# Kernel tuning notes

Measured on AMD Instinct MI355X. Metric: run time of the kernel, lower is better.

Reference implementation:

```python
import jax, jax.numpy as jnp
import numpy as np

DIM = 1024
EPS = 1e-5

def layernorm(x, g, b):
    m = jnp.mean(x, axis=-1, keepdims=True)
    v = jnp.var(x, axis=-1, keepdims=True)
    return (x - m) / jnp.sqrt(v + EPS) * g + b

def setup_inputs() -> dict:
    key = jax.random.key(0)
    ks = jax.random.split(key, 12)
    B, L, D = 4, 2048, DIM
    s = 1.0 / np.sqrt(D)
    return {
        "q": jax.random.normal(ks[0], (B, L, D), jnp.float32),
        "k": jax.random.normal(ks[1], (B, L, D), jnp.float32),
        "v": jax.random.normal(ks[2], (B, L, D), jnp.float32),
        "gq": jnp.ones((D,), jnp.float32), "bq": jnp.zeros((D,), jnp.float32),
        "gk": jnp.ones((D,), jnp.float32), "bk": jnp.zeros((D,), jnp.float32),
        "gv": jnp.ones((D,), jnp.float32), "bv": jnp.zeros((D,), jnp.float32),
        "Wq": jax.random.uniform(ks[3], (D, D), jnp.float32, -s, s),
        "Wk": jax.random.uniform(ks[4], (D, D), jnp.float32, -s, s),
        "Wv": jax.random.uniform(ks[5], (D, D), jnp.float32, -s, s),
        "Wp": jax.random.uniform(ks[6], (D, D), jnp.float32, -s, s),
        "bp": jax.random.uniform(ks[7], (D,), jnp.float32, -s, s),
    }

def reference(q, k, v, gq, bq, gk, bk, gv, bv, Wq, Wk, Wv, Wp, bp):
    scale = DIM ** -0.5
    qn = layernorm(q, gq, bq) @ Wq.T  # [B,Q,D]
    kn = layernorm(k, gk, bk) @ Wk.T  # [B,K,D]
    vn = layernorm(v, gv, bv) @ Wv.T  # [B,K,D]
    attn = jnp.einsum('bqc,bkc->bqk', qn, kn)
    attn = jax.nn.relu(attn) * scale  # ReLU on raw scores, then scale (matches in-place *=)
    attn_mask = jax.nn.softmax(attn, axis=-1)
    out = jnp.einsum('bqk,bkc->bqc', attn_mask, vn)
    out = out @ Wp.T + bp
    return (attn, out)
```

## Files before the change

### kernel.cpp

```cpp
#include <hip/hip_runtime.h>


typedef __attribute__((ext_vector_type(8))) short short8v;
typedef __attribute__((ext_vector_type(4))) float f32x4;

#define DEVI __device__ __forceinline__

DEVI float b2f(unsigned short u) {
  union { unsigned int i; float f; } x;
  x.i = ((unsigned int)u) << 16;
  return x.f;
}
DEVI unsigned short f2b(float f) {
  union { float f; unsigned int i; } x;
  x.f = f;
  unsigned int r = x.i + 0x7fffu + ((x.i >> 16) & 1u);
  return (unsigned short)(r >> 16);
}

DEVI bool sniff_bf16(const unsigned short* wq) {
  int bad = 0;
#pragma unroll
  for (int j = 0; j < 64; ++j) bad |= (fabsf(b2f(wq[j])) > 0.0625f) ? 1 : 0;
  return bad == 0;
}

DEVI void async16(const unsigned short* g, unsigned short* l) {
  __builtin_amdgcn_global_load_lds(
      (const __attribute__((address_space(1))) void*)g,
      (__attribute__((address_space(3))) void*)l, 16, 0, 0);
}

DEVI void wait_lgkm0() { asm volatile("s_waitcnt lgkmcnt(0)" ::: "memory"); }
DEVI void wait_lgkm8() { asm volatile("s_waitcnt lgkmcnt(8)" ::: "memory"); }
template <int N> DEVI void wait_vm();
template <> DEVI void wait_vm<0>() { asm volatile("s_waitcnt vmcnt(0)" ::: "memory"); }
template <> DEVI void wait_vm<6>() { asm volatile("s_waitcnt vmcnt(6)" ::: "memory"); }

DEVI void stage_q(const unsigned short* G, int ld, unsigned short* L,
                  int w, int lane, int k0) {
  int r8 = lane >> 3;
  int scol = ((lane & 7) ^ r8) * 8;
  async16(G + (size_t)(w * 8 + r8) * ld + k0 + scol, L + (w * 8) * 64);
}
DEVI void stage_half(const unsigned short* G, int ld, unsigned short* L,
                     int w, int lane, int k0) {
  stage_q(G, ld, L, w, lane, k0);
  stage_q(G + (size_t)64 * ld, ld, L + 64 * 64, w, lane, k0);
}

template <int NB>
DEVI void gemm8_core(unsigned short* sA, unsigned short* sB,
                     const unsigned short* Ab, const unsigned short* Bb,
                     int m0, int n0, int lda, int ldb, int K, int tid,
                     f32x4 (&acc)[8][2 * NB]) {
  int lane = tid & 63, w = tid >> 6;
  int wm = w >> 2, wn = w & 3;
  int l15 = lane & 15, quad = lane >> 4;
  int rxor = l15 & 7;
  int cb0 = (quad ^ rxor) * 8;
  int cb1 = ((4 + quad) ^ rxor) * 8;
  const int nst = K >> 6;
  const int BSZ = NB * 128 * 64;
  const unsigned short* A_ = Ab + (size_t)m0 * lda;
  const unsigned short* B_ = Bb + (size_t)n0 * ldb;

  if constexpr (NB == 2) {
    const unsigned short* A0 = A_;
    const unsigned short* A1 = A_ + (size_t)128 * lda;
    const unsigned short* B0g = B_;
    const unsigned short* B1g = B_ + (size_t)128 * ldb;
    stage_half(A0, lda, sA, w, lane, 0);
    stage_half(A1, lda, sA + 8192, w, lane, 0);
    stage_half(B0g, ldb, sB, w, lane, 0);
    stage_half(B1g, ldb, sB + 8192, w, lane, 0);
    if (nst > 1) {
      stage_half(A0, lda, sA + 16384, w, lane, 64);
      stage_half(A1, lda, sA + 16384 + 8192, w, lane, 64);
      stage_half(B0g, ldb, sB + 16384, w, lane, 64);
      wait_vm<6>();
    } else {
      wait_vm<0>();
    }
    __builtin_amdgcn_s_barrier();

    for (int t = 0; t < nst; ++t) {
      const int b = t & 1, nb2 = b ^ 1;
      const unsigned short* rA = sA + b * 16384 + (wm * 128 + l15) * 64;
      const unsigned short* rB = sB + b * 16384 + (wn * 64 + l15) * 64;
      short8v a03[4][2], a47[4][2], b01[2][2], b23[2][2];

#pragma unroll
      for (int mt = 0; mt < 4; ++mt) {
        a03[mt][0] = *(const short8v*)(rA + mt * 1024 + cb0);
        a03[mt][1] = *(const short8v*)(rA + mt * 1024 + cb1);
      }
#pragma unroll
      for (int nt = 0; nt < 2; ++nt) {
        b01[nt][0] = *(const short8v*)(rB + nt * 1024 + cb0);
        b01[nt][1] = *(const short8v*)(rB + nt * 1024 + cb1);
      }
      if (t + 1 < nst)
        stage_half(B1g, ldb, sB + nb2 * 16384 + 8192, w, lane, (t + 1) << 6);
      wait_lgkm8();
      __builtin_amdgcn_s_barrier();
      wait_lgkm0();
      __builtin_amdgcn_sched_barrier(0);
      __builtin_amdgcn_s_setprio(1);
#pragma unroll
      for (int mt = 0; mt < 4; ++mt)
#pragma unroll
        for (int nt = 0; nt < 2; ++nt) {
          acc[mt][nt] = __builtin_amdgcn_mfma_f32_16x16x32_bf16(a03[mt][0], b01[nt][0], acc[mt][nt], 0, 0, 0);
          acc[mt][nt] = __builtin_amdgcn_mfma_f32_16x16x32_bf16(a03[mt][1], b01[nt][1], acc[mt][nt], 0, 0, 0);
        }
      __builtin_amdgcn_s_setprio(0);
      __builtin_amdgcn_s_barrier();

#pragma unroll
      for (int mt = 0; mt < 4; ++mt) {
        a47[mt][0] = *(const short8v*)(rA + (4 + mt) * 1024 + cb0);
        a47[mt][1] = *(const short8v*)(rA + (4 + mt) * 1024 + cb1);
      }
      __builtin_amdgcn_s_barrier();
      wait_lgkm0();
      __builtin_amdgcn_sched_barrier(0);
      __builtin_amdgcn_s_setprio(1);
#pragma unroll
      for (int mt = 0; mt < 4; ++mt)
#pragma unroll
        for (int nt = 0; nt < 2; ++nt) {
          acc[4 + mt][nt] = __builtin_amdgcn_mfma_f32_16x16x32_bf16(a47[mt][0], b01[nt][0], acc[4 + mt][nt], 0, 0, 0);
          acc[4 + mt][nt] = __builtin_amdgcn_mfma_f32_16x16x32_bf16(a47[mt][1], b01[nt][1], acc[4 + mt][nt], 0, 0, 0);
        }
      __builtin_amdgcn_s_setprio(0);
      __builtin_amdgcn_s_barrier();

#pragma unroll
      for (int nt = 0; nt < 2; ++nt) {
        b23[nt][0] = *(const short8v*)(rB + (2 + nt) * 1024 + cb0);
        b23[nt][1] = *(const short8v*)(rB + (2 + nt) * 1024 + cb1);
      }
      if (t + 2 < nst)
        stage_half(A0, lda, sA + b * 16384, w, lane, (t + 2) << 6);
      __builtin_amdgcn_s_barrier();
      wait_lgkm0();
      __builtin_amdgcn_sched_barrier(0);
      __builtin_amdgcn_s_setprio(1);
#pragma unroll
      for (int mt = 0; mt < 4; ++mt)
#pragma unroll
        for (int nt = 0; nt < 2; ++nt) {
          acc[mt][2 + nt] = __builtin_amdgcn_mfma_f32_16x16x32_bf16(a03[mt][0], b23[nt][0], acc[mt][2 + nt], 0, 0, 0);
          acc[mt][2 + nt] = __builtin_amdgcn_mfma_f32_16x16x32_bf16(a03[mt][1], b23[nt][1], acc[mt][2 + nt], 0, 0, 0);
        }
      __builtin_amdgcn_s_setprio(0);
      __builtin_amdgcn_s_barrier();

      if (t + 2 < nst) {
        stage_half(A1, lda, sA + b * 16384 + 8192, w, lane, (t + 2) << 6);
        stage_half(B0g, ldb, sB + b * 16384, w, lane, (t + 2) << 6);
      }
      __builtin_amdgcn_s_setprio(1);
#pragma unroll
      for (int mt = 0; mt < 4; ++mt)
#pragma unroll
        for (int nt = 0; nt < 2; ++nt) {
          acc[4 + mt][2 + nt] = __builtin_amdgcn_mfma_f32_16x16x32_bf16(a47[mt][0], b23[nt][0], acc[4 + mt][2 + nt], 0, 0, 0);
          acc[4 + mt][2 + nt] = __builtin_amdgcn_mfma_f32_16x16x32_bf16(a47[mt][1], b23[nt][1], acc[4 + mt][2 + nt], 0, 0, 0);
        }
      __builtin_amdgcn_s_setprio(0);
      if (t + 2 < nst) wait_vm<6>();
      else if (t + 1 < nst) wait_vm<0>();
      __builtin_amdgcn_s_barrier();
    }
  } else {
    stage_q(A_, lda, sA, w, lane, 0);
    stage_q(A_ + (size_t)128 * lda, lda, sA + 128 * 64, w, lane, 0);
    stage_half(B_, ldb, sB, w, lane, 0);
    stage_q(A_ + (size_t)64 * lda, lda, sA + 64 * 64, w, lane, 0);
    stage_q(A_ + (size_t)192 * lda, lda, sA + 192 * 64, w, lane, 0);
    if (nst > 1) {
      stage_q(A_, lda, sA + 16384, w, lane, 64);
      stage_q(A_ + (size_t)128 * lda, lda, sA + 16384 + 128 * 64, w, lane, 64);
      stage_half(B_, ldb, sB + BSZ, w, lane, 64);
    }
    for (int t = 0; t < nst; ++t) {
      const int b = t & 1;
      const unsigned short* rA = sA + b * 16384 + (wm * 128 + l15) * 64;
      const unsigned short* rB = sB + b * BSZ + (wn * 32 + l15) * 64;
      short8v a[4][2], bb[2][2];
      if (t + 1 < nst) {
        int kn = (t + 1) << 6;
        stage_q(A_ + (size_t)64 * lda, lda, sA + (b ^ 1) * 16384 + 64 * 64, w, lane, kn);
        stage_q(A_ + (size_t)192 * lda, lda, sA + (b ^ 1) * 16384 + 192 * 64, w, lane, kn);
        wait_vm<6>();
      } else {
        wait_vm<0>();
      }
      __builtin_amdgcn_s_barrier();
#pragma unroll
      for (int mt = 0; mt < 4; ++mt) {
        a[mt][0] = *(const short8v*)(rA + mt * 1024 + cb0);
        a[mt][1] = *(const short8v*)(rA + mt * 1024 + cb1);
      }
#pragma unroll
      for (int nt = 0; nt < 2; ++nt) {
        bb[nt][0] = *(const short8v*)(rB + nt * 1024 + cb0);
        bb[nt][1] = *(const short8v*)(rB + nt * 1024 + cb1);
      }
      wait_lgkm0();
      __builtin_amdgcn_sched_barrier(0);
      __builtin_amdgcn_s_setprio(1);
#pragma unroll
      for (int mt = 0; mt < 4; ++mt)
#pragma unroll
        for (int nt = 0; nt < 2; ++nt) {
          acc[mt][nt] = __builtin_amdgcn_mfma_f32_16x16x32_bf16(a[mt][0], bb[nt][0], acc[mt][nt], 0, 0, 0);
          acc[mt][nt] = __builtin_amdgcn_mfma_f32_16x16x32_bf16(a[mt][1], bb[nt][1], acc[mt][nt], 0, 0, 0);
        }
      __builtin_amdgcn_s_setprio(0);
      __builtin_amdgcn_s_barrier();
#pragma unroll
      for (int mt = 0; mt < 4; ++mt) {
        a[mt][0] = *(const short8v*)(rA + (4 + mt) * 1024 + cb0);
        a[mt][1] = *(const short8v*)(rA + (4 + mt) * 1024 + cb1);
      }
      if (t + 2 < nst) {
        int kn2 = (t + 2) << 6;
        stage_q(A_, lda, sA + b * 16384, w, lane, kn2);
        stage_q(A_ + (size_t)128 * lda, lda, sA + b * 16384 + 128 * 64, w, lane, kn2);
        stage_half(B_, ldb, sB + b * BSZ, w, lane, kn2);
      }
      __builtin_amdgcn_s_barrier();
      wait_lgkm0();
      __builtin_amdgcn_sched_barrier(0);
      __builtin_amdgcn_s_setprio(1);
#pragma unroll
      for (int mt = 0; mt < 4; ++mt)
#pragma unroll
        for (int nt = 0; nt < 2; ++nt) {
          acc[4 + mt][nt] = __builtin_amdgcn_mfma_f32_16x16x32_bf16(a[mt][0], bb[nt][0], acc[4 + mt][nt], 0, 0, 0);
          acc[4 + mt][nt] = __builtin_amdgcn_mfma_f32_16x16x32_bf16(a[mt][1], bb[nt][1], acc[4 + mt][nt], 0, 0, 0);
        }
      __builtin_amdgcn_s_setprio(0);
      __builtin_amdgcn_s_barrier();
    }
  }
}

DEVI int xcd_swz(int f, int nb) { return (f & 7) * (nb >> 3) + (f >> 3); }

struct PrepArgs {
  const void* q; const void* k; const void* v;
  const void* g[3]; const void* b[3];
  const void* W[4];
};

__global__ __launch_bounds__(256) void k_prep(PrepArgs pa,
    unsigned short* __restrict__ Wb, unsigned short* __restrict__ XN) {
  bool isbf = sniff_bf16((const unsigned short*)pa.W[0]);
  int bid = blockIdx.x, tid = threadIdx.x;
  if (bid < 2048) {
    int s = bid >> 9;
    size_t inner = ((size_t)(bid & 511)) * 2048 + (size_t)tid * 8;
    unsigned short* dst = Wb + (size_t)s * 1048576 + inner;
    if (isbf) {
      *(uint4*)dst = *(const uint4*)((const unsigned short*)pa.W[s] + inner);
    } else {
      const float* f = (const float*)pa.W[s] + inner;
      float4 a = *(const float4*)f;
      float4 b = *(const float4*)(f + 4);
      ushort4 o0 = { f2b(a.x), f2b(a.y), f2b(a.z), f2b(a.w) };
      ushort4 o1 = { f2b(b.x), f2b(b.y), f2b(b.z), f2b(b.w) };
      *(ushort4*)dst = o0;
      *(ushort4*)(dst + 4) = o1;
    }
  } else {
    int rb = bid - 2048;
    int wv = tid >> 6, lane = tid & 63;
    int row = rb * 4 + wv;
    int t = row >> 13;
    size_t r = (size_t)(row & 8191);
    const void* src = (t == 0) ? pa.q : (t == 1) ? pa.k : pa.v;
    float x[16];
    if (isbf) {
      const unsigned short* s = (const unsigned short*)src + r * 1024;
#pragma unroll
      for (int j = 0; j < 2; ++j) {
        uint4 pk = *(const uint4*)(s + j * 512 + lane * 8);
        const unsigned short* ps = (const unsigned short*)&pk;
#pragma unroll
        for (int e = 0; e < 8; ++e) x[j * 8 + e] = b2f(ps[e]);
      }
    } else {
      const float* s = (const float*)src + r * 1024;
#pragma unroll
      for (int j = 0; j < 4; ++j) {
        float4 pk = *(const float4*)(s + j * 256 + lane * 4);
        x[j * 4 + 0] = pk.x; x[j * 4 + 1] = pk.y;
        x[j * 4 + 2] = pk.z; x[j * 4 + 3] = pk.w;
      }
    }
    float s1 = 0.f, s2 = 0.f;
#pragma unroll
    for (int e = 0; e < 16; ++e) { s1 += x[e]; s2 += x[e] * x[e]; }
    for (int off = 32; off > 0; off >>= 1) {
      s1 += __shfl_xor(s1, off);
      s2 += __shfl_xor(s2, off);
    }
    float m  = s1 * (1.0f / 1024.0f);
    float m2 = s2 * (1.0f / 1024.0f);
    float rstd = rsqrtf(m2 - m * m + 1e-5f);
    unsigned short* dst = XN + (size_t)row * 1024;
    if (isbf) {
      const unsigned short* gp = (const unsigned short*)pa.g[t];
      const unsigned short* bp = (const unsigned short*)pa.b[t];
#pragma unroll
      for (int j = 0; j < 2; ++j) {
        uint4 gk = *(const uint4*)(gp + j * 512 + lane * 8);
        uint4 bk = *(const uint4*)(bp + j * 512 + lane * 8);
        const unsigned short* gs = (const unsigned short*)&gk;
        const unsigned short* bs = (const unsigned short*)&bk;
        uint4 out;
        unsigned short* os = (unsigned short*)&out;
#pragma unroll
        for (int e = 0; e < 8; ++e)
          os[e] = f2b((x[j * 8 + e] - m) * rstd * b2f(gs[e]) + b2f(bs[e]));
        *(uint4*)(dst + j * 512 + lane * 8) = out;
      }
    } else {
      const float* gp = (const float*)pa.g[t];
      const float* bp = (const float*)pa.b[t];
#pragma unroll
      for (int j = 0; j < 4; ++j) {
        float4 gk = *(const float4*)(gp + j * 256 + lane * 4);
        float4 bk = *(const float4*)(bp + j * 256 + lane * 4);
        ushort4 o;
        o.x = f2b((x[j * 4 + 0] - m) * rstd * gk.x + bk.x);
        o.y = f2b((x[j * 4 + 1] - m) * rstd * gk.y + bk.y);
        o.z = f2b((x[j * 4 + 2] - m) * rstd * gk.z + bk.z);
        o.w = f2b((x[j * 4 + 3] - m) * rstd * gk.w + bk.w);
        *(ushort4*)(dst + j * 256 + lane * 4) = o;
      }
    }
  }
}

__global__ __launch_bounds__(512, 2) void k_megaproj(
    const unsigned short* __restrict__ XN, const unsigned short* __restrict__ Wb,
    unsigned short* __restrict__ QN, unsigned short* __restrict__ VNT) {
  __shared__ __align__(16) unsigned short sA[2 * 256 * 64];
  __shared__ __align__(16) unsigned short sB[2 * 256 * 64];
  int x = xcd_swz((int)blockIdx.x, 384), tid = threadIdx.x;
  int lane = tid & 63, w = tid >> 6;
  int wm = w >> 2, wn = w & 3;
  int l15 = lane & 15, quad = lane >> 4;
  f32x4 acc[8][4];
#pragma unroll
  for (int i = 0; i < 8; ++i)
#pragma unroll
    for (int j = 0; j < 4; ++j) acc[i][j] = (f32x4){0.f, 0.f, 0.f, 0.f};

  unsigned short* C;
  int m0, n0, ldc;
  if (x < 256) {
    int t = x >> 7, i = x & 127;
    m0 = (i >> 2) * 256; n0 = (i & 3) * 256; ldc = 1024;
    gemm8_core<2>(sA, sB, XN + (size_t)t * 8388608, Wb + (size_t)t * 1048576,
                  m0, n0, 1024, 1024, 1024, tid, acc);
    C = QN + (size_t)t * 8388608;
  } else {
    int i = x - 256, z = i >> 5, j = i & 31;
    m0 = (j >> 3) * 256; n0 = (j & 7) * 256; ldc = 2048;
    gemm8_core<2>(sA, sB, Wb + 2 * 1048576, XN + 2 * 8388608 + (size_t)z * 2097152,
                  m0, n0, 1024, 1024, 1024, tid, acc);
    C = VNT + (size_t)z * 2097152;
  }
#pragma unroll
  for (int mt = 0; mt < 8; ++mt) {
    int mb = m0 + wm * 128 + mt * 16 + quad * 4;
#pragma unroll
    for (int nt = 0; nt < 4; ++nt) {
      int n = n0 + wn * 64 + nt * 16 + l15;
      f32x4 vc = acc[mt][nt];
#pragma unroll
      for (int r2 = 0; r2 < 4; ++r2) C[(size_t)(mb + r2) * ldc + n] = f2b(vc[r2]);
    }
  }
}

template <int EPI, int NB>
__global__ __launch_bounds__(512, 2) void k_gemm(
    const unsigned short* __restrict__ A, const unsigned short* __restrict__ B,
    void* __restrict__ Cv, long long coff,
    int K, int lda, int ldb, int ldc,
    long long sAb, long long sBb, long long sCb,
    float scale, const void* __restrict__ bias,
    const unsigned short* __restrict__ wq_sniff) {
  __shared__ __align__(16) unsigned short sA[2 * 256 * 64];
  __shared__ __align__(16) unsigned short sB[2 * NB * 128 * 64];
  int tid = threadIdx.x;
  int lane = tid & 63, w = tid >> 6;
  int wm = w >> 2, wn = w & 3;
  int l15 = lane & 15, quad = lane >> 4;

  int gx = gridDim.x, gy = gridDim.y;
  int nb = gx * gy * (int)gridDim.z;
  int f = (int)blockIdx.x + gx * ((int)blockIdx.y + gy * (int)blockIdx.z);
  f = xcd_swz(f, nb);
  int bx = f % gx;
  int rem = f / gx;
  int by = rem % gy;
  int bz = rem / gy;

  int m0 = by * 256, n0 = bx * (NB * 128);
  f32x4 acc[8][2 * NB];
#pragma unroll
  for (int i = 0; i < 8; ++i)
#pragma unroll
    for (int j = 0; j < 2 * NB; ++j) acc[i][j] = (f32x4){0.f, 0.f, 0.f, 0.f};

  gemm8_core<NB>(sA, sB, A + (long long)bz * sAb, B + (long long)bz * sBb,
                 m0, n0, lda, ldb, K, tid, acc);

  long long cbase = coff + (long long)bz * sCb;
  bool isbf = (EPI != 0) ? sniff_bf16(wq_sniff) : true;
#pragma unroll
  for (int mt = 0; mt < 8; ++mt) {
    int mb = m0 + wm * 128 + mt * 16 + quad * 4;
#pragma unroll
    for (int nt = 0; nt < 2 * NB; ++nt) {
      int n = n0 + wn * (NB * 32) + nt * 16 + l15;
      f32x4 vc = acc[mt][nt];
      if (EPI == 0) {
        unsigned short* C = (unsigned short*)Cv + cbase;
#pragma unroll
        for (int r2 = 0; r2 < 4; ++r2) C[(size_t)(mb + r2) * ldc + n] = f2b(vc[r2]);
      } else if (EPI == 1) {
        if (isbf) {
          unsigned short* C = (unsigned short*)Cv + cbase;
#pragma unroll
          for (int r2 = 0; r2 < 4; ++r2)
            C[(size_t)(mb + r2) * ldc + n] = f2b(fmaxf(vc[r2], 0.f) * scale);
        } else {
          float* C = (float*)Cv + cbase;
#pragma unroll
          for (int r2 = 0; r2 < 4; ++r2)
            C[(size_t)(mb + r2) * ldc + n] = fmaxf(vc[r2], 0.f) * scale;
        }
      } else {
        float bv2 = isbf ? b2f(((const unsigned short*)bias)[n])
                         : ((const float*)bias)[n];
        if (isbf) {
          unsigned short* C = (unsigned short*)Cv + cbase;
#pragma unroll
          for (int r2 = 0; r2 < 4; ++r2) C[(size_t)(mb + r2) * ldc + n] = f2b(vc[r2] + bv2);
        } else {
          float* C = (float*)Cv + cbase;
#pragma unroll
          for (int r2 = 0; r2 < 4; ++r2) C[(size_t)(mb + r2) * ldc + n] = vc[r2] + bv2;
        }
      }
    }
  }
}

__global__ __launch_bounds__(256) void k_softmax(const void* __restrict__ S,
    unsigned short* __restrict__ P, const unsigned short* __restrict__ wq_sniff) {
  bool isbf = sniff_bf16(wq_sniff);
  size_t row = blockIdx.x;
  int tid = threadIdx.x;
  float v[8];
  if (isbf) {
    const unsigned short* s = (const unsigned short*)S + row * 2048 + (size_t)tid * 8;
    ushort4 a = *(const ushort4*)s;
    ushort4 b = *(const ushort4*)(s + 4);
    v[0] = b2f(a.x); v[1] = b2f(a.y); v[2] = b2f(a.z); v[3] = b2f(a.w);
    v[4] = b2f(b.x); v[5] = b2f(b.y); v[6] = b2f(b.z); v[7] = b2f(b.w);
  } else {
    const float* s = (const float*)S + row * 2048 + (size_t)tid * 8;
    float4 a = *(const float4*)s;
    float4 b = *(const float4*)(s + 4);
    v[0] = a.x; v[1] = a.y; v[2] = a.z; v[3] = a.w;
    v[4] = b.x; v[5] = b.y; v[6] = b.z; v[7] = b.w;
  }
  float mx = v[0];
#pragma unroll
  for (int j = 1; j < 8; ++j) mx = fmaxf(mx, v[j]);
  for (int off = 32; off > 0; off >>= 1) mx = fmaxf(mx, __shfl_down(mx, off));
  __shared__ float sh[8];
  if ((tid & 63) == 0) sh[tid >> 6] = mx;
  __syncthreads();
  mx = fmaxf(fmaxf(sh[0], sh[1]), fmaxf(sh[2], sh[3]));
  float sum = 0.f;
#pragma unroll
  for (int j = 0; j < 8; ++j) { v[j] = __expf(v[j] - mx); sum += v[j]; }
  for (int off = 32; off > 0; off >>= 1) sum += __shfl_down(sum, off);
  if ((tid & 63) == 0) sh[4 + (tid >> 6)] = sum;
  __syncthreads();
  float inv = 1.0f / (sh[4] + sh[5] + sh[6] + sh[7]);
  ushort4 o0 = { f2b(v[0] * inv), f2b(v[1] * inv), f2b(v[2] * inv), f2b(v[3] * inv) };
  ushort4 o1 = { f2b(v[4] * inv), f2b(v[5] * inv), f2b(v[6] * inv), f2b(v[7] * inv) };
  unsigned short* p = P + row * 2048 + (size_t)tid * 8;
  *(ushort4*)p = o0;
  *(ushort4*)(p + 4) = o1;
}

static const size_t MB_ = 1024 * 1024;
static const size_t OFF_W   = 0;
static const size_t OFF_XN  = 8 * MB_ + 128 * 1024;
static const size_t OFF_QN  = OFF_XN + 48 * MB_;
static const size_t OFF_VNT = OFF_QN + 32 * MB_;
static const size_t OFF_P   = OFF_XN;
static const size_t OFF_O1  = OFF_XN + 32 * MB_;

extern "C" void kernel_launch(void* const* d_in, const int* in_sizes, int n_in,
                              void* d_out, int out_size, void* d_ws, size_t ws_size,
                              hipStream_t stream) {
  (void)in_sizes; (void)n_in; (void)out_size; (void)ws_size;
  char* ws = (char*)d_ws;
  unsigned short* Wb  = (unsigned short*)(ws + OFF_W);
  unsigned short* XN  = (unsigned short*)(ws + OFF_XN);
  unsigned short* QN  = (unsigned short*)(ws + OFF_QN);
  unsigned short* VNT = (unsigned short*)(ws + OFF_VNT);
  unsigned short* P   = (unsigned short*)(ws + OFF_P);
  unsigned short* O1  = (unsigned short*)(ws + OFF_O1);
  const unsigned short* WqS = (const unsigned short*)d_in[9];

  PrepArgs pa;
  pa.q = d_in[0]; pa.k = d_in[1]; pa.v = d_in[2];
  pa.g[0] = d_in[3]; pa.b[0] = d_in[4];
  pa.g[1] = d_in[5]; pa.b[1] = d_in[6];
  pa.g[2] = d_in[7]; pa.b[2] = d_in[8];
  pa.W[0] = d_in[9]; pa.W[1] = d_in[10]; pa.W[2] = d_in[11]; pa.W[3] = d_in[12];

  k_prep<<<8192, 256, 0, stream>>>(pa, Wb, XN);

  k_megaproj<<<384, 512, 0, stream>>>(XN, Wb, QN, VNT);

  k_gemm<1, 2><<<dim3(8, 8, 4), 512, 0, stream>>>(
      QN, QN + 8388608, d_out,
      0,
      1024, 1024, 1024, 2048,
      2097152LL, 2097152LL, 4194304LL,
      0.03125f, nullptr, WqS);

  k_softmax<<<8192, 256, 0, stream>>>(d_out, P, WqS);

  k_gemm<0, 1><<<dim3(8, 8, 4), 512, 0, stream>>>(
      P, VNT, O1,
      0,
      2048, 2048, 2048, 1024,
      4194304LL, 2097152LL, 2097152LL,
      0.f, nullptr, WqS);

  k_gemm<3, 1><<<dim3(8, 32, 1), 512, 0, stream>>>(
      O1, Wb + 3 * 1048576, d_out,
      16777216,
      1024, 1024, 1024, 1024,
      0LL, 0LL, 0LL,
      0.f, d_in[13], WqS);
}
```

Measured before the change: 404.4 us.

## Restructure GEMM main loop into single-barrier prefetch pipeline and split V projection tiles

Rewrites the shared gemm8_core software pipeline so each k-step issues the next stage's global-to-LDS loads up front, uses partial lgkmcnt waits between MFMA groups, and needs only one workgroup barrier per iteration instead of many. It also preloads the next stage's first fragments before the final MFMA block to hide LDS latency. Separately, the V projection in k_megaproj now uses 256x128 tiles (NB=1), raising its block count so the grid grows to 512 blocks, with XCD swizzle applied per branch. The risk is more register pressure from holding next-stage fragments, and less slack for the loads to land, since the loop waits for all outstanding loads (vmcnt 0) before its barrier each step.

```diff
diff --git a/kernel.cpp b/kernel.cpp
--- a/kernel.cpp
+++ b/kernel.cpp
@@ -31,11 +31,15 @@
       (__attribute__((address_space(3))) void*)l, 16, 0, 0);
 }
 
-DEVI void wait_lgkm0() { asm volatile("s_waitcnt lgkmcnt(0)" ::: "memory"); }
-DEVI void wait_lgkm8() { asm volatile("s_waitcnt lgkmcnt(8)" ::: "memory"); }
+template <int N> DEVI void wait_lgkm();
+template <> DEVI void wait_lgkm<0>() { asm volatile("s_waitcnt lgkmcnt(0)" ::: "memory"); }
+template <> DEVI void wait_lgkm<4>() { asm volatile("s_waitcnt lgkmcnt(4)" ::: "memory"); }
+template <> DEVI void wait_lgkm<8>() { asm volatile("s_waitcnt lgkmcnt(8)" ::: "memory"); }
 template <int N> DEVI void wait_vm();
 template <> DEVI void wait_vm<0>() { asm volatile("s_waitcnt vmcnt(0)" ::: "memory"); }
 template <> DEVI void wait_vm<6>() { asm volatile("s_waitcnt vmcnt(6)" ::: "memory"); }
+template <> DEVI void wait_vm<8>() { asm volatile("s_waitcnt vmcnt(8)" ::: "memory"); }
+#define SB0() __builtin_amdgcn_sched_barrier(0)
 
 DEVI void stage_q(const unsigned short* G, int ld, unsigned short* L,
                   int w, int lane, int k0) {
@@ -61,91 +65,103 @@
   int cb0 = (quad ^ rxor) * 8;
   int cb1 = ((4 + quad) ^ rxor) * 8;
   const int nst = K >> 6;
-  const int BSZ = NB * 128 * 64;
-  const unsigned short* A_ = Ab + (size_t)m0 * lda;
-  const unsigned short* B_ = Bb + (size_t)n0 * ldb;
-
-  if constexpr (NB == 2) {
-    const unsigned short* A0 = A_;
-    const unsigned short* A1 = A_ + (size_t)128 * lda;
-    const unsigned short* B0g = B_;
-    const unsigned short* B1g = B_ + (size_t)128 * ldb;
-    stage_half(A0, lda, sA, w, lane, 0);
-    stage_half(A1, lda, sA + 8192, w, lane, 0);
-    stage_half(B0g, ldb, sB, w, lane, 0);
-    stage_half(B1g, ldb, sB + 8192, w, lane, 0);
-    if (nst > 1) {
-      stage_half(A0, lda, sA + 16384, w, lane, 64);
-      stage_half(A1, lda, sA + 16384 + 8192, w, lane, 64);
-      stage_half(B0g, ldb, sB + 16384, w, lane, 64);
+  const int ABUF = 16384;
+  const int BBUF = NB * 128 * 64;
+  const unsigned short* A0 = Ab + (size_t)m0 * lda;
+  const unsigned short* A1 = A0 + (size_t)128 * lda;
+  const unsigned short* B0 = Bb + (size_t)n0 * ldb;
+  const unsigned short* B1 = B0 + (size_t)128 * ldb;
+
+  stage_half(A0, lda, sA, w, lane, 0);
+  stage_half(A1, lda, sA + 8192, w, lane, 0);
+  stage_half(B0, ldb, sB, w, lane, 0);
+  if constexpr (NB == 2) stage_half(B1, ldb, sB + 8192, w, lane, 0);
+  if (nst > 1) {
+    stage_half(A0, lda, sA + ABUF, w, lane, 64);
+    stage_half(A1, lda, sA + ABUF + 8192, w, lane, 64);
+    stage_half(B0, ldb, sB + BBUF, w, lane, 64);
+    if constexpr (NB == 2) {
+      stage_half(B1, ldb, sB + BBUF + 8192, w, lane, 64);
+      wait_vm<8>();
+    } else {
       wait_vm<6>();
-    } else {
-      wait_vm<0>();
-    }
-    __builtin_amdgcn_s_barrier();
-
-    for (int t = 0; t < nst; ++t) {
-      const int b = t & 1, nb2 = b ^ 1;
-      const unsigned short* rA = sA + b * 16384 + (wm * 128 + l15) * 64;
-      const unsigned short* rB = sB + b * 16384 + (wn * 64 + l15) * 64;
-      short8v a03[4][2], a47[4][2], b01[2][2], b23[2][2];
-
-#pragma unroll
-      for (int mt = 0; mt < 4; ++mt) {
-        a03[mt][0] = *(const short8v*)(rA + mt * 1024 + cb0);
-        a03[mt][1] = *(const short8v*)(rA + mt * 1024 + cb1);
-      }
-#pragma unroll
-      for (int nt = 0; nt < 2; ++nt) {
-        b01[nt][0] = *(const short8v*)(rB + nt * 1024 + cb0);
-        b01[nt][1] = *(const short8v*)(rB + nt * 1024 + cb1);
-      }
-      if (t + 1 < nst)
-        stage_half(B1g, ldb, sB + nb2 * 16384 + 8192, w, lane, (t + 1) << 6);
-      wait_lgkm8();
-      __builtin_amdgcn_s_barrier();
-      wait_lgkm0();
-      __builtin_amdgcn_sched_barrier(0);
-      __builtin_amdgcn_s_setprio(1);
-#pragma unroll
-      for (int mt = 0; mt < 4; ++mt)
-#pragma unroll
-        for (int nt = 0; nt < 2; ++nt) {
-          acc[mt][nt] = __builtin_amdgcn_mfma_f32_16x16x32_bf16(a03[mt][0], b01[nt][0], acc[mt][nt], 0, 0, 0);
-          acc[mt][nt] = __builtin_amdgcn_mfma_f32_16x16x32_bf16(a03[mt][1], b01[nt][1], acc[mt][nt], 0, 0, 0);
-        }
-      __builtin_amdgcn_s_setprio(0);
-      __builtin_amdgcn_s_barrier();
-
+    }
+  } else {
+    wait_vm<0>();
+  }
+  __builtin_amdgcn_s_barrier();
+  SB0();
+
+  short8v a03[4][2], a47[4][2], b01[2][2], b23[2][2];
+  {
+    const unsigned short* rA = sA + (wm * 128 + l15) * 64;
+    const unsigned short* rB = sB + (wn * (NB * 32) + l15) * 64;
+#pragma unroll
+    for (int mt = 0; mt < 4; ++mt) {
+      a03[mt][0] = *(const short8v*)(rA + mt * 1024 + cb0);
+      a03[mt][1] = *(const short8v*)(rA + mt * 1024 + cb1);
+    }
+#pragma unroll
+    for (int nt = 0; nt < 2; ++nt) {
+      b01[nt][0] = *(const short8v*)(rB + nt * 1024 + cb0);
+      b01[nt][1] = *(const short8v*)(rB + nt * 1024 + cb1);
+    }
+  }
+
+  for (int t = 0; t < nst; ++t) {
+    const int b = t & 1;
+    const bool st = (t + 1 < nst);
+    const int kn = (t + 1) << 6;
+    const unsigned short* rA = sA + b * ABUF + (wm * 128 + l15) * 64;
+    const unsigned short* rB = sB + b * BBUF + (wn * (NB * 32) + l15) * 64;
+    const unsigned short* rAn = sA + (b ^ 1) * ABUF + (wm * 128 + l15) * 64;
+    const unsigned short* rBn = sB + (b ^ 1) * BBUF + (wn * (NB * 32) + l15) * 64;
+
+    if constexpr (NB == 2) {
+      if (st) {
+        stage_half(A0, lda, sA + (b ^ 1) * ABUF, w, lane, kn);
+        stage_half(A1, lda, sA + (b ^ 1) * ABUF + 8192, w, lane, kn);
+      }
 #pragma unroll
       for (int mt = 0; mt < 4; ++mt) {
         a47[mt][0] = *(const short8v*)(rA + (4 + mt) * 1024 + cb0);
         a47[mt][1] = *(const short8v*)(rA + (4 + mt) * 1024 + cb1);
       }
-      __builtin_amdgcn_s_barrier();
-      wait_lgkm0();
-      __builtin_amdgcn_sched_barrier(0);
+      wait_lgkm<8>();
+      SB0();
       __builtin_amdgcn_s_setprio(1);
 #pragma unroll
       for (int mt = 0; mt < 4; ++mt)
 #pragma unroll
         for (int nt = 0; nt < 2; ++nt) {
-          acc[4 + mt][nt] = __builtin_amdgcn_mfma_f32_16x16x32_bf16(a47[mt][0], b01[nt][0], acc[4 + mt][nt], 0, 0, 0);
-          acc[4 + mt][nt] = __builtin_amdgcn_mfma_f32_16x16x32_bf16(a47[mt][1], b01[nt][1], acc[4 + mt][nt], 0, 0, 0);
+          acc[mt][nt] = __builtin_amdgcn_mfma_f32_16x16x32_bf16(a03[mt][0], b01[nt][0], acc[mt][nt], 0, 0, 0);
+          acc[mt][nt] = __builtin_amdgcn_mfma_f32_16x16x32_bf16(a03[mt][1], b01[nt][1], acc[mt][nt], 0, 0, 0);
         }
       __builtin_amdgcn_s_setprio(0);
-      __builtin_amdgcn_s_barrier();
-
+
+      if (st) {
+        stage_half(B0, ldb, sB + (b ^ 1) * BBUF, w, lane, kn);
+        stage_half(B1, ldb, sB + (b ^ 1) * BBUF + 8192, w, lane, kn);
+      }
 #pragma unroll
       for (int nt = 0; nt < 2; ++nt) {
         b23[nt][0] = *(const short8v*)(rB + (2 + nt) * 1024 + cb0);
         b23[nt][1] = *(const short8v*)(rB + (2 + nt) * 1024 + cb1);
       }
-      if (t + 2 < nst)
-        stage_half(A0, lda, sA + b * 16384, w, lane, (t + 2) << 6);
-      __builtin_amdgcn_s_barrier();
-      wait_lgkm0();
-      __builtin_amdgcn_sched_barrier(0);
+      wait_lgkm<4>();
+      SB0();
+      __builtin_amdgcn_s_setprio(1);
+#pragma unroll
+      for (int mt = 0; mt < 4; ++mt)
+#pragma unroll
+        for (int nt = 0; nt < 2; ++nt) {
+          acc[4 + mt][nt] = __builtin_amdgcn_mfma_f32_16x16x32_bf16(a47[mt][0], b01[nt][0], acc[4 + mt][nt], 0, 0, 0);
+          acc[4 + mt][nt] = __builtin_amdgcn_mfma_f32_16x16x32_bf16(a47[mt][1], b01[nt][1], acc[4 + mt][nt], 0, 0, 0);
+        }
+      __builtin_amdgcn_s_setprio(0);
+
+      wait_lgkm<0>();
+      SB0();
       __builtin_amdgcn_s_setprio(1);
 #pragma unroll
       for (int mt = 0; mt < 4; ++mt)
@@ -155,11 +171,21 @@
           acc[mt][2 + nt] = __builtin_amdgcn_mfma_f32_16x16x32_bf16(a03[mt][1], b23[nt][1], acc[mt][2 + nt], 0, 0, 0);
         }
       __builtin_amdgcn_s_setprio(0);
-      __builtin_amdgcn_s_barrier();
-
-      if (t + 2 < nst) {
-        stage_half(A1, lda, sA + b * 16384 + 8192, w, lane, (t + 2) << 6);
-        stage_half(B0g, ldb, sB + b * 16384, w, lane, (t + 2) << 6);
+
+      if (st) {
+        wait_vm<0>();
+        __builtin_amdgcn_s_barrier();
+        SB0();
+#pragma unroll
+        for (int mt = 0; mt < 4; ++mt) {
+          a03[mt][0] = *(const short8v*)(rAn + mt * 1024 + cb0);
+          a03[mt][1] = *(const short8v*)(rAn + mt * 1024 + cb1);
+        }
+#pragma unroll
+        for (int nt = 0; nt < 2; ++nt) {
+          b01[nt][0] = *(const short8v*)(rBn + nt * 1024 + cb0);
+          b01[nt][1] = *(const short8v*)(rBn + nt * 1024 + cb1);
+        }
       }
       __builtin_amdgcn_s_setprio(1);
 #pragma unroll
@@ -170,81 +196,57 @@
           acc[4 + mt][2 + nt] = __builtin_amdgcn_mfma_f32_16x16x32_bf16(a47[mt][1], b23[nt][1], acc[4 + mt][2 + nt], 0, 0, 0);
         }
       __builtin_amdgcn_s_setprio(0);
-      if (t + 2 < nst) wait_vm<6>();
-      else if (t + 1 < nst) wait_vm<0>();
-      __builtin_amdgcn_s_barrier();
-    }
-  } else {
-    stage_q(A_, lda, sA, w, lane, 0);
-    stage_q(A_ + (size_t)128 * lda, lda, sA + 128 * 64, w, lane, 0);
-    stage_half(B_, ldb, sB, w, lane, 0);
-    stage_q(A_ + (size_t)64 * lda, lda, sA + 64 * 64, w, lane, 0);
-    stage_q(A_ + (size_t)192 * lda, lda, sA + 192 * 64, w, lane, 0);
-    if (nst > 1) {
-      stage_q(A_, lda, sA + 16384, w, lane, 64);
-      stage_q(A_ + (size_t)128 * lda, lda, sA + 16384 + 128 * 64, w, lane, 64);
-      stage_half(B_, ldb, sB + BSZ, w, lane, 64);
-    }
-    for (int t = 0; t < nst; ++t) {
-      const int b = t & 1;
-      const unsigned short* rA = sA + b * 16384 + (wm * 128 + l15) * 64;
-      const unsigned short* rB = sB + b * BSZ + (wn * 32 + l15) * 64;
-      short8v a[4][2], bb[2][2];
-      if (t + 1 < nst) {
-        int kn = (t + 1) << 6;
-        stage_q(A_ + (size_t)64 * lda, lda, sA + (b ^ 1) * 16384 + 64 * 64, w, lane, kn);
-        stage_q(A_ + (size_t)192 * lda, lda, sA + (b ^ 1) * 16384 + 192 * 64, w, lane, kn);
-        wait_vm<6>();
-      } else {
+    } else {
+      if (st) {
+        stage_half(A0, lda, sA + (b ^ 1) * ABUF, w, lane, kn);
+        stage_half(A1, lda, sA + (b ^ 1) * ABUF + 8192, w, lane, kn);
+        stage_half(B0, ldb, sB + (b ^ 1) * BBUF, w, lane, kn);
+      }
+#pragma unroll
+      for (int mt = 0; mt < 4; ++mt) {
+        a47[mt][0] = *(const short8v*)(rA + (4 + mt) * 1024 + cb0);
+        a47[mt][1] = *(const short8v*)(rA + (4 + mt) * 1024 + cb1);
+      }
+      wait_lgkm<8>();
+      SB0();
+      __builtin_amdgcn_s_setprio(1);
+#pragma unroll
+      for (int mt = 0; mt < 4; ++mt)
+#pragma unroll
+        for (int nt = 0; nt < 2; ++nt) {
+          acc[mt][nt] = __builtin_amdgcn_mfma_f32_16x16x32_bf16(a03[mt][0], b01[nt][0], acc[mt][nt], 0, 0, 0);
+          acc[mt][nt] = __builtin_amdgcn_mfma_f32_16x16x32_bf16(a03[mt][1], b01[nt][1], acc[mt][nt], 0, 0, 0);
+        }
+      __builtin_amdgcn_s_setprio(0);
+
+      wait_lgkm<0>();
+      SB0();
+      if (st) {
         wait_vm<0>();
-      }
-      __builtin_amdgcn_s_barrier();
-#pragma unroll
-      for (int mt = 0; mt < 4; ++mt) {
-        a[mt][0] = *(const short8v*)(rA + mt * 1024 + cb0);
-        a[mt][1] = *(const short8v*)(rA + mt * 1024 + cb1);
-      }
-#pragma unroll
-      for (int nt = 0; nt < 2; ++nt) {
-        bb[nt][0] = *(const short8v*)(rB + nt * 1024 + cb0);
-        bb[nt][1] = *(const short8v*)(rB + nt * 1024 + cb1);
-      }
-      wait_lgkm0();
-      __builtin_amdgcn_sched_barrier(0);
+        __builtin_amdgcn_s_barrier();
+        SB0();
+#pragma unroll
+        for (int mt = 0; mt < 4; ++mt) {
+          a03[mt][0] = *(const short8v*)(rAn + mt * 1024 + cb0);
+          a03[mt][1] = *(const short8v*)(rAn + mt * 1024 + cb1);
+        }
+      }
       __builtin_amdgcn_s_setprio(1);
 #pragma unroll
       for (int mt = 0; mt < 4; ++mt)
 #pragma unroll
         for (int nt = 0; nt < 2; ++nt) {
-          acc[mt][nt] = __builtin_amdgcn_mfma_f32_16x16x32_bf16(a[mt][0], bb[nt][0], acc[mt][nt], 0, 0, 0);
-          acc[mt][nt] = __builtin_amdgcn_mfma_f32_16x16x32_bf16(a[mt][1], bb[nt][1], acc[mt][nt], 0, 0, 0);
+          acc[4 + mt][nt] = __builtin_amdgcn_mfma_f32_16x16x32_bf16(a47[mt][0], b01[nt][0], acc[4 + mt][nt], 0, 0, 0);
+          acc[4 + mt][nt] = __builtin_amdgcn_mfma_f32_16x16x32_bf16(a47[mt][1], b01[nt][1], acc[4 + mt][nt], 0, 0, 0);
         }
       __builtin_amdgcn_s_setprio(0);
-      __builtin_amdgcn_s_barrier();
-#pragma unroll
-      for (int mt = 0; mt < 4; ++mt) {
-        a[mt][0] = *(const short8v*)(rA + (4 + mt) * 1024 + cb0);
-        a[mt][1] = *(const short8v*)(rA + (4 + mt) * 1024 + cb1);
-      }
-      if (t + 2 < nst) {
-        int kn2 = (t + 2) << 6;
-        stage_q(A_, lda, sA + b * 16384, w, lane, kn2);
-        stage_q(A_ + (size_t)128 * lda, lda, sA + b * 16384 + 128 * 64, w, lane, kn2);
-        stage_half(B_, ldb, sB + b * BSZ, w, lane, kn2);
-      }
-      __builtin_amdgcn_s_barrier();
-      wait_lgkm0();
-      __builtin_amdgcn_sched_barrier(0);
-      __builtin_amdgcn_s_setprio(1);
-#pragma unroll
-      for (int mt = 0; mt < 4; ++mt)
-#pragma unroll
-        for (int nt = 0; nt < 2; ++nt) {
-          acc[4 + mt][nt] = __builtin_amdgcn_mfma_f32_16x16x32_bf16(a[mt][0], bb[nt][0], acc[4 + mt][nt], 0, 0, 0);
-          acc[4 + mt][nt] = __builtin_amdgcn_mfma_f32_16x16x32_bf16(a[mt][1], bb[nt][1], acc[4 + mt][nt], 0, 0, 0);
-        }
-      __builtin_amdgcn_s_setprio(0);
-      __builtin_amdgcn_s_barrier();
+      if (st) {
+#pragma unroll
+        for (int nt = 0; nt < 2; ++nt) {
+          b01[nt][0] = *(const short8v*)(rBn + nt * 1024 + cb0);
+          b01[nt][1] = *(const short8v*)(rBn + nt * 1024 + cb1);
+        }
+      }
     }
   }
 }
@@ -352,40 +354,56 @@
     unsigned short* __restrict__ QN, unsigned short* __restrict__ VNT) {
   __shared__ __align__(16) unsigned short sA[2 * 256 * 64];
   __shared__ __align__(16) unsigned short sB[2 * 256 * 64];
-  int x = xcd_swz((int)blockIdx.x, 384), tid = threadIdx.x;
+  int x = blockIdx.x, tid = threadIdx.x;
   int lane = tid & 63, w = tid >> 6;
   int wm = w >> 2, wn = w & 3;
   int l15 = lane & 15, quad = lane >> 4;
-  f32x4 acc[8][4];
-#pragma unroll
-  for (int i = 0; i < 8; ++i)
-#pragma unroll
-    for (int j = 0; j < 4; ++j) acc[i][j] = (f32x4){0.f, 0.f, 0.f, 0.f};
-
-  unsigned short* C;
-  int m0, n0, ldc;
+
   if (x < 256) {
-    int t = x >> 7, i = x & 127;
-    m0 = (i >> 2) * 256; n0 = (i & 3) * 256; ldc = 1024;
+    int i = xcd_swz(x, 256);
+    int t = i >> 7, j = i & 127;
+    int m0 = (j >> 2) * 256, n0 = (j & 3) * 256;
+    f32x4 acc[8][4];
+#pragma unroll
+    for (int a = 0; a < 8; ++a)
+#pragma unroll
+      for (int c = 0; c < 4; ++c) acc[a][c] = (f32x4){0.f, 0.f, 0.f, 0.f};
     gemm8_core<2>(sA, sB, XN + (size_t)t * 8388608, Wb + (size_t)t * 1048576,
                   m0, n0, 1024, 1024, 1024, tid, acc);
-    C = QN + (size_t)t * 8388608;
+    unsigned short* C = QN + (size_t)t * 8388608;
+#pragma unroll
+    for (int mt = 0; mt < 8; ++mt) {
+      int mb = m0 + wm * 128 + mt * 16 + quad * 4;
+#pragma unroll
+      for (int nt = 0; nt < 4; ++nt) {
+        int n = n0 + wn * 64 + nt * 16 + l15;
+        f32x4 vc = acc[mt][nt];
+#pragma unroll
+        for (int r2 = 0; r2 < 4; ++r2) C[(size_t)(mb + r2) * 1024 + n] = f2b(vc[r2]);
+      }
+    }
   } else {
-    int i = x - 256, z = i >> 5, j = i & 31;
-    m0 = (j >> 3) * 256; n0 = (j & 7) * 256; ldc = 2048;
-    gemm8_core<2>(sA, sB, Wb + 2 * 1048576, XN + 2 * 8388608 + (size_t)z * 2097152,
+    int i = xcd_swz(x - 256, 256);
+    int z = i >> 6, j = i & 63;
+    int m0 = (j >> 4) * 256, n0 = (j & 15) * 128;
+    f32x4 acc[8][2];
+#pragma unroll
+    for (int a = 0; a < 8; ++a)
+#pragma unroll
+      for (int c = 0; c < 2; ++c) acc[a][c] = (f32x4){0.f, 0.f, 0.f, 0.f};
+    gemm8_core<1>(sA, sB, Wb + 2 * 1048576, XN + 2 * 8388608 + (size_t)z * 2097152,
                   m0, n0, 1024, 1024, 1024, tid, acc);
-    C = VNT + (size_t)z * 2097152;
-  }
-#pragma unroll
-  for (int mt = 0; mt < 8; ++mt) {
-    int mb = m0 + wm * 128 + mt * 16 + quad * 4;
-#pragma unroll
-    for (int nt = 0; nt < 4; ++nt) {
-      int n = n0 + wn * 64 + nt * 16 + l15;
-      f32x4 vc = acc[mt][nt];
-#pragma unroll
-      for (int r2 = 0; r2 < 4; ++r2) C[(size_t)(mb + r2) * ldc + n] = f2b(vc[r2]);
+    unsigned short* C = VNT + (size_t)z * 2097152;
+#pragma unroll
+    for (int mt = 0; mt < 8; ++mt) {
+      int mb = m0 + wm * 128 + mt * 16 + quad * 4;
+#pragma unroll
+      for (int nt = 0; nt < 2; ++nt) {
+        int n = n0 + wn * 32 + nt * 16 + l15;
+        f32x4 vc = acc[mt][nt];
+#pragma unroll
+        for (int r2 = 0; r2 < 4; ++r2) C[(size_t)(mb + r2) * 2048 + n] = f2b(vc[r2]);
+      }
     }
   }
 }
@@ -537,7 +555,7 @@
 
   k_prep<<<8192, 256, 0, stream>>>(pa, Wb, XN);
 
-  k_megaproj<<<384, 512, 0, stream>>>(XN, Wb, QN, VNT);
+  k_megaproj<<<512, 512, 0, stream>>>(XN, Wb, QN, VNT);
 
   k_gemm<1, 2><<<dim3(8, 8, 4), 512, 0, stream>>>(
       QN, QN + 8388608, d_out,
```

New measurement: 385.0 us. 1.05x faster.
